# Kernel optimization log

Hardware: AMD Instinct MI355X
Metric: run time of the kernel (lower is better)

Reference implementation:

```python
import jax, jax.numpy as jnp
import numpy as np

B, S, E, H = 4, 2048, 1024, 16
D = E // H  # head_size = 64

def setup_inputs() -> dict:
    key = jax.random.key(0)
    ks = jax.random.split(key, 10)
    s_e = E ** -0.5
    s_4e = (4 * E) ** -0.5
    inp = {
        "x": jax.random.normal(ks[0], (B, S, E), dtype=jnp.float32),
        # per-head Q/K/V weights, stacked: [H, E, D], no bias
        "Wq": jax.random.normal(ks[1], (H, E, D), dtype=jnp.float32) * s_e,
        "Wk": jax.random.normal(ks[2], (H, E, D), dtype=jnp.float32) * s_e,
        "Wv": jax.random.normal(ks[3], (H, E, D), dtype=jnp.float32) * s_e,
        "Wo": jax.random.normal(ks[4], (E, E), dtype=jnp.float32) * s_e,
        "bo": jax.random.normal(ks[5], (E,), dtype=jnp.float32) * 0.01,
        "W1": jax.random.normal(ks[6], (E, 4 * E), dtype=jnp.float32) * s_e,
        "b1": jax.random.normal(ks[7], (4 * E,), dtype=jnp.float32) * 0.01,
        "W2": jax.random.normal(ks[8], (4 * E, E), dtype=jnp.float32) * s_4e,
        "b2": jax.random.normal(ks[9], (E,), dtype=jnp.float32) * 0.01,
    }
    return inp

def reference(x, Wq, Wk, Wv, Wo, bo, W1, b1, W2, b2):
    b, s, e = x.shape
    # NOTE: original scales by embedding_size**-0.5 (Size of x), not head_size
    scale = e ** -0.5
    q = jnp.einsum("bse,hed->bhsd", x, Wq)
    k = jnp.einsum("bse,hed->bhsd", x, Wk)
    v = jnp.einsum("bse,hed->bhsd", x, Wv)
    scores = jnp.einsum("bhsd,bhtd->bhst", q, k) * scale
    causal = jnp.tril(jnp.ones((s, s), dtype=bool))
    scores = jnp.where(causal, scores, -jnp.inf)
    weights = jax.nn.softmax(scores, axis=-1)
    attn = jnp.einsum("bhst,bhtd->bhsd", weights, v)  # [B,H,S,D]
    # concat heads along last dim: [B,S,H*D]
    attn = attn.transpose(0, 2, 1, 3).reshape(b, s, e)
    y = attn @ Wo + bo
    x = x + y  # residual (no LayerNorm applied in original forward)
    h = jax.nn.relu(x @ W1 + b1)
    ffn = h @ W2 + b2
    return x + ffn
```

## Files before the change

kernel.cpp:

```cpp
#include <hip/hip_runtime.h>
#include <stdint.h>

#define B_ 4
#define S_ 2048
#define E_ 1024
#define H_ 16
#define D_ 64

typedef unsigned short u16;
typedef u16 u16x8 __attribute__((ext_vector_type(8)));
typedef __bf16 bf16x8 __attribute__((ext_vector_type(8)));
typedef float f32x4 __attribute__((ext_vector_type(4)));

__device__ __forceinline__ float bf2f(u16 x) {
  unsigned int v = ((unsigned int)x) << 16;
  return __builtin_bit_cast(float, v);
}
__device__ __forceinline__ u16 f2bf(float f) {
  unsigned int u = __builtin_bit_cast(unsigned int, f);
  unsigned int r = (u + 0x7fffu + ((u >> 16) & 1u)) >> 16;
  return (u16)r;
}

__device__ __forceinline__ void gl2lds16(const u16* g, u16* l) {
  __builtin_amdgcn_global_load_lds(
      (const __attribute__((address_space(1))) void*)g,
      (__attribute__((address_space(3))) void*)l, 16, 0, 0);
}

__global__ __launch_bounds__(256) void cast_bf16_k(const float* __restrict__ src,
                                                   u16* __restrict__ dst, long n) {
  long i = ((long)blockIdx.x * 256 + threadIdx.x) * 8;
  if (i + 8 <= n) {
    f32x4 a = *(const f32x4*)(src + i), b = *(const f32x4*)(src + i + 4);
    u16x8 o;
#pragma unroll
    for (int j = 0; j < 4; j++) { o[j] = f2bf(a[j]); o[j + 4] = f2bf(b[j]); }
    *(u16x8*)(dst + i) = o;
  }
}

__global__ __launch_bounds__(256) void castT_k(const float* __restrict__ src,
                                               u16* __restrict__ dst, int R, int C) {
  long bofs = (long)blockIdx.z * R * C;
  src += bofs; dst += bofs;
  __shared__ u16 t[32][33];
  int c0 = blockIdx.x * 32, r0 = blockIdx.y * 32;
  int lc = threadIdx.x & 31, lr8 = threadIdx.x >> 5;
#pragma unroll
  for (int i = 0; i < 4; i++) {
    int lr = lr8 + i * 8;
    t[lr][lc] = f2bf(src[(long)(r0 + lr) * C + c0 + lc]);
  }
  __syncthreads();
#pragma unroll
  for (int i = 0; i < 4; i++) {
    int lr = lr8 + i * 8;
    dst[(long)(c0 + lr) * R + r0 + lc] = t[lc][lr];
  }
}

__global__ __launch_bounds__(256) void vT_k(const u16* __restrict__ QKV,
                                            u16* __restrict__ VTg) {
  int bh = blockIdx.z, d0 = blockIdx.y * 32, t0 = blockIdx.x * 32;
  int b = bh >> 4, h = bh & 15;
  __shared__ u16 t[32][33];
  int lc = threadIdx.x & 31, lr8 = threadIdx.x >> 5;
#pragma unroll
  for (int i = 0; i < 4; i++) {
    int lr = lr8 + i * 8;
    t[lr][lc] = QKV[(long)(b * S_ + t0 + lr) * 3072 + 2048 + h * 64 + d0 + lc];
  }
  __syncthreads();
#pragma unroll
  for (int i = 0; i < 4; i++) {
    int lr = lr8 + i * 8;
    VTg[((long)bh * 64 + d0 + lr) * S_ + t0 + lc] = t[lc][lr];
  }
}

template <bool AF32, bool CF32>
__global__ __launch_bounds__(256) void gemm128(const void* __restrict__ Av,
                                               const u16* __restrict__ BT,
                                               void* __restrict__ Cv,
                                               const float* __restrict__ bias,
                                               const float* __restrict__ resid,
                                               int M, int N, int K, int relu,
                                               u16* __restrict__ Cbf) {
  __shared__ u16 As[128 * 32];
  __shared__ u16 Bs[128 * 32];
  const int tid = threadIdx.x;
  const int wave = tid >> 6, lane = tid & 63;
  const int m0 = blockIdx.y * 128, n0 = blockIdx.x * 128;
  const int wm = wave >> 1, wn = wave & 1;
  const int fr = lane & 15, quad = lane >> 4;

  f32x4 acc[4][4] = {};

  const int srow = wave * 32 + (lane >> 2);
  const int skcol = (lane & 3) * 8;

  for (int k0 = 0; k0 < K; k0 += 32) {
    __syncthreads();
    if (AF32) {
      const float* Ap = (const float*)Av + (long)(m0 + (tid >> 1)) * K + k0 + (tid & 1) * 16;
      f32x4 f0 = *(const f32x4*)Ap, f1 = *(const f32x4*)(Ap + 4);
      f32x4 f2 = *(const f32x4*)(Ap + 8), f3 = *(const f32x4*)(Ap + 12);
      u16x8 p0, p1;
#pragma unroll
      for (int j = 0; j < 4; j++) {
        p0[j] = f2bf(f0[j]); p0[j + 4] = f2bf(f1[j]);
        p1[j] = f2bf(f2[j]); p1[j + 4] = f2bf(f3[j]);
      }
      *(u16x8*)&As[(tid >> 1) * 32 + (tid & 1) * 16] = p0;
      *(u16x8*)&As[(tid >> 1) * 32 + (tid & 1) * 16 + 8] = p1;
    } else {
      const u16* Ag = (const u16*)Av + (long)(m0 + srow) * K + k0 + skcol;
      gl2lds16(Ag, &As[(wave * 32) * 32]);
      gl2lds16(Ag + 16 * (long)K, &As[(wave * 32 + 16) * 32]);
    }
    {
      const u16* Bg = BT + (long)(n0 + srow) * K + k0 + skcol;
      gl2lds16(Bg, &Bs[(wave * 32) * 32]);
      gl2lds16(Bg + 16 * (long)K, &Bs[(wave * 32 + 16) * 32]);
    }
    __syncthreads();

    bf16x8 af[4], bfr[4];
#pragma unroll
    for (int mi = 0; mi < 4; mi++)
      af[mi] = __builtin_bit_cast(bf16x8, *(const u16x8*)&As[(wm * 64 + mi * 16 + fr) * 32 + quad * 8]);
#pragma unroll
    for (int ni = 0; ni < 4; ni++)
      bfr[ni] = __builtin_bit_cast(bf16x8, *(const u16x8*)&Bs[(wn * 64 + ni * 16 + fr) * 32 + quad * 8]);
#pragma unroll
    for (int mi = 0; mi < 4; mi++)
#pragma unroll
      for (int ni = 0; ni < 4; ni++)
        acc[mi][ni] = __builtin_amdgcn_mfma_f32_16x16x32_bf16(af[mi], bfr[ni], acc[mi][ni], 0, 0, 0);
  }

#pragma unroll
  for (int mi = 0; mi < 4; mi++)
#pragma unroll
    for (int ni = 0; ni < 4; ni++)
#pragma unroll
      for (int r = 0; r < 4; r++) {
        int gm = m0 + wm * 64 + mi * 16 + quad * 4 + r;
        int gn = n0 + wn * 64 + ni * 16 + fr;
        float v = acc[mi][ni][r];
        if (bias) v += bias[gn];
        if (resid) v += resid[(long)gm * N + gn];
        if (relu) v = fmaxf(v, 0.f);
        if (CF32) ((float*)Cv)[(long)gm * N + gn] = v;
        else      ((u16*)Cv)[(long)gm * N + gn] = f2bf(v);
        if (Cbf) Cbf[(long)gm * N + gn] = f2bf(v);
      }
}

__device__ __forceinline__ bf16x8 ldfrag32(const u16* base, int r, int quad) {
  int u = (r * 32 + quad * 8) ^ (((r >> 3) & 1) << 4);
  return __builtin_bit_cast(bf16x8, *(const u16x8*)(base + u));
}

__device__ __forceinline__ void stage_tile(const u16* __restrict__ A,
                                           const u16* __restrict__ BT, int K,
                                           int m0, int n0, int k0,
                                           u16* __restrict__ buf,
                                           int sr_, int sc_, int wbase) {
#pragma unroll
  for (int h = 0; h < 2; h++) {
    int r = h * 128 + sr_;
    int c = sc_ ^ (((r >> 3) & 1) << 4);
    gl2lds16(A + (size_t)(m0 + r) * K + k0 + c, buf + h * 4096 + wbase);
  }
  int c = sc_ ^ (((sr_ >> 3) & 1) << 4);
  gl2lds16(BT + (size_t)(n0 + sr_) * K + k0 + c, buf + 8192 + wbase);
}

template <bool CF32>
__global__ __launch_bounds__(512) void gemm3b(const u16* __restrict__ A,
                                              const u16* __restrict__ BT,
                                              void* __restrict__ Cv,
                                              const float* __restrict__ bias,
                                              const float* __restrict__ resid,
                                              int M, int N, int K, int relu,
                                              u16* __restrict__ Cbf) {
  (void)M;
  constexpr int BM = 256, BN = 128, BK = 32;
  constexpr int AU = BM * BK;
  constexpr int BUF = AU + BN * BK;

  __shared__ u16 sm[3 * BUF];
  const int tid = threadIdx.x;
  const int wave = tid >> 6, lane = tid & 63;
  const int wm = wave >> 1, wn = wave & 1;
  const int fr = lane & 15, quad = lane >> 4;

  const int nbx = gridDim.x;
  const int nwg = nbx * (int)gridDim.y;
  const int wgid = blockIdx.y * nbx + blockIdx.x;
  const int qq = nwg >> 3, rr = nwg & 7;
  const int xcd = wgid & 7, loc = wgid >> 3;
  const int sw = (xcd < rr ? xcd * (qq + 1) : rr * (qq + 1) + (xcd - rr) * qq) + loc;
  const int n0 = (sw % nbx) * BN;
  const int m0 = (sw / nbx) * BM;

  const int NT = K / BK;

  f32x4 acc[4][4] = {};

  const int sc_ = (tid & 3) * 8;
  const int sr_ = tid >> 2;
  const int wbase = wave << 9;

  const int rA = wm * 64 + fr;
  const int rB = wn * 64 + fr;

  stage_tile(A, BT, K, m0, n0, 0, sm, sr_, sc_, wbase);
  if (NT > 1) {
    stage_tile(A, BT, K, m0, n0, BK, sm + BUF, sr_, sc_, wbase);
    asm volatile("s_waitcnt vmcnt(3)" ::: "memory");
  } else {
    asm volatile("s_waitcnt vmcnt(0)" ::: "memory");
  }
  __builtin_amdgcn_s_barrier();

  int cur = 0;
  for (int t = 0; t < NT; ++t) {
    u16* cb = sm + cur * BUF;

    if (t + 2 < NT) {
      int s2 = cur + 2; if (s2 >= 3) s2 -= 3;
      stage_tile(A, BT, K, m0, n0, (t + 2) * BK, sm + s2 * BUF, sr_, sc_, wbase);
    }

    bf16x8 aF[4], bF[4];
#pragma unroll
    for (int mi = 0; mi < 4; ++mi) aF[mi] = ldfrag32(cb, rA + mi * 16, quad);
#pragma unroll
    for (int ni = 0; ni < 4; ++ni) bF[ni] = ldfrag32(cb + AU, rB + ni * 16, quad);

    asm volatile("s_waitcnt lgkmcnt(0)" ::: "memory");
    __builtin_amdgcn_sched_barrier(0);
    __builtin_amdgcn_s_setprio(1);
#pragma unroll
    for (int mi = 0; mi < 4; ++mi)
#pragma unroll
      for (int ni = 0; ni < 4; ++ni)
        acc[mi][ni] = __builtin_amdgcn_mfma_f32_16x16x32_bf16(aF[mi], bF[ni], acc[mi][ni], 0, 0, 0);
    __builtin_amdgcn_s_setprio(0);

    if (t + 2 < NT) asm volatile("s_waitcnt vmcnt(3)" ::: "memory");
    else            asm volatile("s_waitcnt vmcnt(0)" ::: "memory");
    __builtin_amdgcn_s_barrier();
    cur = cur + 1; if (cur >= 3) cur -= 3;
  }

#pragma unroll
  for (int mi = 0; mi < 4; ++mi)
#pragma unroll
    for (int ni = 0; ni < 4; ++ni)
#pragma unroll
      for (int r = 0; r < 4; ++r) {
        int gm = m0 + wm * 64 + mi * 16 + quad * 4 + r;
        int gn = n0 + wn * 64 + ni * 16 + fr;
        float v = acc[mi][ni][r];
        if (bias) v += bias[gn];
        if (resid) v += resid[(long)gm * N + gn];
        if (relu) v = fmaxf(v, 0.f);
        if (CF32) ((float*)Cv)[(long)gm * N + gn] = v;
        else      ((u16*)Cv)[(long)gm * N + gn] = f2bf(v);
        if (Cbf) Cbf[(long)gm * N + gn] = f2bf(v);
      }
}

__device__ __forceinline__ void stage_tile_s(const u16* __restrict__ A,
                                             const u16* __restrict__ BT, int K,
                                             int m0, int n0, int k0,
                                             u16* __restrict__ buf,
                                             int sr_, int sc_, int wbase) {
#pragma unroll
  for (int h = 0; h < 2; h++) {
    int r = h * 64 + sr_;
    int c = sc_ ^ (((r >> 3) & 1) << 4);
    gl2lds16(A + (size_t)(m0 + r) * K + k0 + c, buf + h * 2048 + wbase);
  }
#pragma unroll
  for (int h = 0; h < 2; h++) {
    int r = h * 64 + sr_;
    int c = sc_ ^ (((r >> 3) & 1) << 4);
    gl2lds16(BT + (size_t)(n0 + r) * K + k0 + c, buf + 4096 + h * 2048 + wbase);
  }
}

template <bool CF32>
__global__ __launch_bounds__(256) void gemm3s(const u16* __restrict__ A,
                                              const u16* __restrict__ BT,
                                              void* __restrict__ Cv,
                                              const float* __restrict__ bias,
                                              const float* __restrict__ resid,
                                              int M, int N, int K, int relu,
                                              u16* __restrict__ Cbf) {
  (void)M;
  constexpr int BM = 128, BN = 128, BK = 32;
  constexpr int AU = BM * BK;
  constexpr int BUF = 2 * AU;

  __shared__ u16 sm[3 * BUF];
  const int tid = threadIdx.x;
  const int wave = tid >> 6, lane = tid & 63;
  const int wm = wave >> 1, wn = wave & 1;
  const int fr = lane & 15, quad = lane >> 4;

  const int nbx = gridDim.x;
  const int nwg = nbx * (int)gridDim.y;
  const int wgid = blockIdx.y * nbx + blockIdx.x;
  const int qq = nwg >> 3, rr = nwg & 7;
  const int xcd = wgid & 7, loc = wgid >> 3;
  const int sw = (xcd < rr ? xcd * (qq + 1) : rr * (qq + 1) + (xcd - rr) * qq) + loc;
  const int n0 = (sw % nbx) * BN;
  const int m0 = (sw / nbx) * BM;

  const int NT = K / BK;

  f32x4 acc[4][4] = {};

  const int sc_ = (tid & 3) * 8;
  const int sr_ = tid >> 2;
  const int wbase = wave << 9;

  const int rA = wm * 64 + fr;
  const int rB = wn * 64 + fr;

  stage_tile_s(A, BT, K, m0, n0, 0, sm, sr_, sc_, wbase);
  if (NT > 1) {
    stage_tile_s(A, BT, K, m0, n0, BK, sm + BUF, sr_, sc_, wbase);
    asm volatile("s_waitcnt vmcnt(4)" ::: "memory");
  } else {
    asm volatile("s_waitcnt vmcnt(0)" ::: "memory");
  }
  __builtin_amdgcn_s_barrier();

  int cur = 0;
  for (int t = 0; t < NT; ++t) {
    u16* cb = sm + cur * BUF;

    if (t + 2 < NT) {
      int s2 = cur + 2; if (s2 >= 3) s2 -= 3;
      stage_tile_s(A, BT, K, m0, n0, (t + 2) * BK, sm + s2 * BUF, sr_, sc_, wbase);
    }

    bf16x8 aF[4], bF[4];
#pragma unroll
    for (int mi = 0; mi < 4; ++mi) aF[mi] = ldfrag32(cb, rA + mi * 16, quad);
#pragma unroll
    for (int ni = 0; ni < 4; ++ni) bF[ni] = ldfrag32(cb + AU, rB + ni * 16, quad);

    asm volatile("s_waitcnt lgkmcnt(0)" ::: "memory");
    __builtin_amdgcn_sched_barrier(0);
    __builtin_amdgcn_s_setprio(1);
#pragma unroll
    for (int mi = 0; mi < 4; ++mi)
#pragma unroll
      for (int ni = 0; ni < 4; ++ni)
        acc[mi][ni] = __builtin_amdgcn_mfma_f32_16x16x32_bf16(aF[mi], bF[ni], acc[mi][ni], 0, 0, 0);
    __builtin_amdgcn_s_setprio(0);

    if (t + 2 < NT) asm volatile("s_waitcnt vmcnt(4)" ::: "memory");
    else            asm volatile("s_waitcnt vmcnt(0)" ::: "memory");
    __builtin_amdgcn_s_barrier();
    cur = cur + 1; if (cur >= 3) cur -= 3;
  }

#pragma unroll
  for (int mi = 0; mi < 4; ++mi)
#pragma unroll
    for (int ni = 0; ni < 4; ++ni)
#pragma unroll
      for (int r = 0; r < 4; ++r) {
        int gm = m0 + wm * 64 + mi * 16 + quad * 4 + r;
        int gn = n0 + wn * 64 + ni * 16 + fr;
        float v = acc[mi][ni][r];
        if (bias) v += bias[gn];
        if (resid) v += resid[(long)gm * N + gn];
        if (relu) v = fmaxf(v, 0.f);
        if (CF32) ((float*)Cv)[(long)gm * N + gn] = v;
        else      ((u16*)Cv)[(long)gm * N + gn] = f2bf(v);
        if (Cbf) Cbf[(long)gm * N + gn] = f2bf(v);
      }
}

#define SWZ(row, col) ((((row) << 6)) + ((col) ^ (((row) & 7) << 3)))

__global__ __launch_bounds__(256) void attn_mfma3(const u16* __restrict__ QKV,
                                                  const u16* __restrict__ VTg,
                                                  u16* __restrict__ attn) {
  int p = blockIdx.x, h = blockIdx.y, b = blockIdx.z;
  int tid = threadIdx.x;
  int wq = tid >> 6, lane = tid & 63;
  int fr = lane & 15, quad = lane >> 4;
  int kf = quad * 8;

  __shared__ u16 Qs[64 * 64];
  __shared__ u16 Ks[64 * 64];
  __shared__ u16 Vt[64 * 64];
  __shared__ u16 Ps[4 * 16 * 64];

  const u16* base = QKV + (long)b * S_ * 3072;
  const u16* vbase = VTg + (long)(b * 16 + h) * 64 * S_;
  int st = tid >> 2;
  int sd = (tid & 3) * 16;

  const float qsc = 0.03125f * 1.4426950408889634f;

  for (int ti = 0; ti < 2; ti++) {
    int qt = ti ? (31 - p) : p;

    {
      const u16* qr = base + (long)(qt * 64 + st) * 3072 + h * 64 + sd;
      u16x8 a = *(const u16x8*)qr, d = *(const u16x8*)(qr + 8);
      u16x8 oa, od;
#pragma unroll
      for (int j = 0; j < 8; j++) {
        oa[j] = f2bf(bf2f(a[j]) * qsc);
        od[j] = f2bf(bf2f(d[j]) * qsc);
      }
      *(u16x8*)&Qs[SWZ(st, sd)] = oa;
      *(u16x8*)&Qs[SWZ(st, sd + 8)] = od;
    }
    __syncthreads();
    bf16x8 qf0 = __builtin_bit_cast(bf16x8, *(const u16x8*)&Qs[SWZ(wq * 16 + fr, kf)]);
    bf16x8 qf1 = __builtin_bit_cast(bf16x8, *(const u16x8*)&Qs[SWZ(wq * 16 + fr, 32 + kf)]);

    f32x4 acc[4] = {};
    float l[4] = {0.f, 0.f, 0.f, 0.f};

    for (int c = 0; c <= qt; c++) {
      int t0 = c * 64;
      __syncthreads();
      {
        const u16* kr = base + (long)(t0 + st) * 3072 + 1024 + h * 64 + sd;
        u16x8 k0 = *(const u16x8*)kr, k1 = *(const u16x8*)(kr + 8);
        const u16* vr = vbase + (long)st * S_ + t0 + sd;
        u16x8 v0 = *(const u16x8*)vr, v1 = *(const u16x8*)(vr + 8);
        *(u16x8*)&Ks[SWZ(st, sd)] = k0;
        *(u16x8*)&Ks[SWZ(st, sd + 8)] = k1;
        *(u16x8*)&Vt[SWZ(st, sd)] = v0;
        *(u16x8*)&Vt[SWZ(st, sd + 8)] = v1;
      }
      __syncthreads();

      f32x4 sc[4] = {};
#pragma unroll
      for (int nt = 0; nt < 4; nt++) {
        bf16x8 b0 = __builtin_bit_cast(bf16x8, *(const u16x8*)&Ks[SWZ(nt * 16 + fr, kf)]);
        bf16x8 b1 = __builtin_bit_cast(bf16x8, *(const u16x8*)&Ks[SWZ(nt * 16 + fr, 32 + kf)]);
        sc[nt] = __builtin_amdgcn_mfma_f32_16x16x32_bf16(qf0, b0, sc[nt], 0, 0, 0);
        sc[nt] = __builtin_amdgcn_mfma_f32_16x16x32_bf16(qf1, b1, sc[nt], 0, 0, 0);
      }

      if (c == qt) {
        int qloc = wq * 16 + quad * 4;
#pragma unroll
        for (int nt = 0; nt < 4; nt++)
#pragma unroll
          for (int r = 0; r < 4; r++)
            if (nt * 16 + fr > qloc + r) sc[nt][r] = -1e30f;
      }

      const int pb = wq << 10;
      const int prow = quad * 4;
#pragma unroll
      for (int nt = 0; nt < 4; nt++) {
        int col = nt * 16 + fr;
#pragma unroll
        for (int r = 0; r < 4; r++) {
          float pv = exp2f(sc[nt][r]);
          l[r] += pv;
          Ps[pb + SWZ(prow + r, col)] = f2bf(pv);
        }
      }

      bf16x8 pa0 = __builtin_bit_cast(bf16x8, *(const u16x8*)&Ps[pb + SWZ(fr, kf)]);
      bf16x8 pa1 = __builtin_bit_cast(bf16x8, *(const u16x8*)&Ps[pb + SWZ(fr, 32 + kf)]);
#pragma unroll
      for (int nt = 0; nt < 4; nt++) {
        bf16x8 vb0 = __builtin_bit_cast(bf16x8, *(const u16x8*)&Vt[SWZ(nt * 16 + fr, kf)]);
        bf16x8 vb1 = __builtin_bit_cast(bf16x8, *(const u16x8*)&Vt[SWZ(nt * 16 + fr, 32 + kf)]);
        acc[nt] = __builtin_amdgcn_mfma_f32_16x16x32_bf16(pa0, vb0, acc[nt], 0, 0, 0);
        acc[nt] = __builtin_amdgcn_mfma_f32_16x16x32_bf16(pa1, vb1, acc[nt], 0, 0, 0);
      }
    }

#pragma unroll
    for (int r = 0; r < 4; r++)
#pragma unroll
      for (int off = 1; off < 16; off <<= 1) l[r] += __shfl_xor(l[r], off);

    long row = (long)b * S_ + qt * 64 + wq * 16 + quad * 4;
#pragma unroll
    for (int nt = 0; nt < 4; nt++)
#pragma unroll
      for (int r = 0; r < 4; r++)
        attn[(row + r) * 1024 + h * 64 + nt * 16 + fr] = f2bf(acc[nt][r] / l[r]);
  }
}

extern "C" void kernel_launch(void* const* d_in, const int* in_sizes, int n_in,
                              void* d_out, int out_size, void* d_ws, size_t ws_size,
                              hipStream_t stream) {
  (void)in_sizes; (void)n_in; (void)out_size;
  const float* x  = (const float*)d_in[0];
  const float* Wq = (const float*)d_in[1];
  const float* Wk = (const float*)d_in[2];
  const float* Wv = (const float*)d_in[3];
  const float* Wo = (const float*)d_in[4];
  const float* bo = (const float*)d_in[5];
  const float* W1 = (const float*)d_in[6];
  const float* b1 = (const float*)d_in[7];
  const float* W2 = (const float*)d_in[8];
  const float* b2 = (const float*)d_in[9];
  float* out = (float*)d_out;

  char* ws = (char*)d_ws;
  u16*   QKV  = (u16*)(ws);
  u16*   attn = (u16*)(ws + 50331648);
  u16*   hbuf = (u16*)(ws);
  float* x1   = (float*)(ws + 67108864);
  u16*   VTg  = (u16*)(ws + 67108864);
  u16*   xb   = (u16*)(ws + 83886080);
  u16*   WT   = (u16*)(ws + 100663296);
  u16*   WoT  = (u16*)(ws + 106954752);
  u16*   W1T  = (u16*)(ws + 109051904);
  u16*   W2T  = (u16*)(ws + 117440512);
  u16*   x1b  = (u16*)(ws + 125829120);
  bool bigws = ws_size >= (size_t)142606336;

  cast_bf16_k<<<4096, 256, 0, stream>>>(x, xb, (long)8192 * 1024);
  castT_k<<<dim3(2, 32, 16), 256, 0, stream>>>(Wq, WT, 1024, 64);
  castT_k<<<dim3(2, 32, 16), 256, 0, stream>>>(Wk, WT + 1048576, 1024, 64);
  castT_k<<<dim3(2, 32, 16), 256, 0, stream>>>(Wv, WT + 2097152, 1024, 64);
  castT_k<<<dim3(32, 32, 1), 256, 0, stream>>>(Wo, WoT, 1024, 1024);
  castT_k<<<dim3(128, 32, 1), 256, 0, stream>>>(W1, W1T, 1024, 4096);
  castT_k<<<dim3(32, 128, 1), 256, 0, stream>>>(W2, W2T, 4096, 1024);

  gemm3s<false><<<dim3(24, 64), 256, 0, stream>>>(xb, WT, QKV, nullptr, nullptr, 8192, 3072, 1024, 0, nullptr);
  vT_k<<<dim3(64, 2, 64), 256, 0, stream>>>(QKV, VTg);
  attn_mfma3<<<dim3(16, H_, B_), 256, 0, stream>>>(QKV, VTg, attn);
  gemm3s<true><<<dim3(8, 64), 256, 0, stream>>>(attn, WoT, x1, bo, x, 8192, 1024, 1024, 0, bigws ? x1b : nullptr);
  if (bigws)
    gemm3b<false><<<dim3(32, 32), 512, 0, stream>>>(x1b, W1T, hbuf, b1, nullptr, 8192, 4096, 1024, 1, nullptr);
  else
    gemm128<true, false><<<dim3(32, 64), 256, 0, stream>>>(x1, W1T, hbuf, b1, nullptr, 8192, 4096, 1024, 1, nullptr);
  gemm3s<true><<<dim3(8, 64), 256, 0, stream>>>(hbuf, W2T, out, b2, x1, 8192, 1024, 4096, 0, nullptr);
}
```

Measured before the change: 569.1 us.

## Use 256x256 GEMM tiles, 256-row tiles elsewhere, padded LDS in attention

Adds a 512-thread GEMM variant with 256x256 block tiles and uses it for the QKV and W1 projections. The Wo and W2 projections move onto the existing 256x128 512-thread kernel. The attention kernel switches from an XOR-swizzled LDS layout to row padding, and from exp2f with the log2e factor folded into Q to __expf. Larger tiles raise operand reuse per block and cut redundant global loads, but they leave fewer blocks per launch, which can hurt wave quantization. The QKV launch, for example, has 384 blocks.

```diff
diff --git a/kernel.cpp b/kernel.cpp
--- a/kernel.cpp
+++ b/kernel.cpp
@@ -275,27 +275,27 @@
       }
 }
 
-__device__ __forceinline__ void stage_tile_s(const u16* __restrict__ A,
+__device__ __forceinline__ void stage_tile_w(const u16* __restrict__ A,
                                              const u16* __restrict__ BT, int K,
                                              int m0, int n0, int k0,
                                              u16* __restrict__ buf,
                                              int sr_, int sc_, int wbase) {
 #pragma unroll
   for (int h = 0; h < 2; h++) {
-    int r = h * 64 + sr_;
+    int r = h * 128 + sr_;
     int c = sc_ ^ (((r >> 3) & 1) << 4);
-    gl2lds16(A + (size_t)(m0 + r) * K + k0 + c, buf + h * 2048 + wbase);
+    gl2lds16(A + (size_t)(m0 + r) * K + k0 + c, buf + h * 4096 + wbase);
   }
 #pragma unroll
   for (int h = 0; h < 2; h++) {
-    int r = h * 64 + sr_;
+    int r = h * 128 + sr_;
     int c = sc_ ^ (((r >> 3) & 1) << 4);
-    gl2lds16(BT + (size_t)(n0 + r) * K + k0 + c, buf + 4096 + h * 2048 + wbase);
+    gl2lds16(BT + (size_t)(n0 + r) * K + k0 + c, buf + 8192 + h * 4096 + wbase);
   }
 }
 
 template <bool CF32>
-__global__ __launch_bounds__(256) void gemm3s(const u16* __restrict__ A,
+__global__ __launch_bounds__(512) void gemm3w(const u16* __restrict__ A,
                                               const u16* __restrict__ BT,
                                               void* __restrict__ Cv,
                                               const float* __restrict__ bias,
@@ -303,14 +303,14 @@
                                               int M, int N, int K, int relu,
                                               u16* __restrict__ Cbf) {
   (void)M;
-  constexpr int BM = 128, BN = 128, BK = 32;
+  constexpr int BM = 256, BN = 256, BK = 32;
   constexpr int AU = BM * BK;
   constexpr int BUF = 2 * AU;
 
   __shared__ u16 sm[3 * BUF];
   const int tid = threadIdx.x;
   const int wave = tid >> 6, lane = tid & 63;
-  const int wm = wave >> 1, wn = wave & 1;
+  const int wm = wave >> 2, wn = wave & 3;
   const int fr = lane & 15, quad = lane >> 4;
 
   const int nbx = gridDim.x;
@@ -324,18 +324,18 @@
 
   const int NT = K / BK;
 
-  f32x4 acc[4][4] = {};
+  f32x4 acc[8][4] = {};
 
   const int sc_ = (tid & 3) * 8;
   const int sr_ = tid >> 2;
   const int wbase = wave << 9;
 
-  const int rA = wm * 64 + fr;
+  const int rA = wm * 128 + fr;
   const int rB = wn * 64 + fr;
 
-  stage_tile_s(A, BT, K, m0, n0, 0, sm, sr_, sc_, wbase);
+  stage_tile_w(A, BT, K, m0, n0, 0, sm, sr_, sc_, wbase);
   if (NT > 1) {
-    stage_tile_s(A, BT, K, m0, n0, BK, sm + BUF, sr_, sc_, wbase);
+    stage_tile_w(A, BT, K, m0, n0, BK, sm + BUF, sr_, sc_, wbase);
     asm volatile("s_waitcnt vmcnt(4)" ::: "memory");
   } else {
     asm volatile("s_waitcnt vmcnt(0)" ::: "memory");
@@ -348,12 +348,12 @@
 
     if (t + 2 < NT) {
       int s2 = cur + 2; if (s2 >= 3) s2 -= 3;
-      stage_tile_s(A, BT, K, m0, n0, (t + 2) * BK, sm + s2 * BUF, sr_, sc_, wbase);
+      stage_tile_w(A, BT, K, m0, n0, (t + 2) * BK, sm + s2 * BUF, sr_, sc_, wbase);
     }
 
-    bf16x8 aF[4], bF[4];
-#pragma unroll
-    for (int mi = 0; mi < 4; ++mi) aF[mi] = ldfrag32(cb, rA + mi * 16, quad);
+    bf16x8 aF[8], bF[4];
+#pragma unroll
+    for (int mi = 0; mi < 8; ++mi) aF[mi] = ldfrag32(cb, rA + mi * 16, quad);
 #pragma unroll
     for (int ni = 0; ni < 4; ++ni) bF[ni] = ldfrag32(cb + AU, rB + ni * 16, quad);
 
@@ -361,7 +361,7 @@
     __builtin_amdgcn_sched_barrier(0);
     __builtin_amdgcn_s_setprio(1);
 #pragma unroll
-    for (int mi = 0; mi < 4; ++mi)
+    for (int mi = 0; mi < 8; ++mi)
 #pragma unroll
       for (int ni = 0; ni < 4; ++ni)
         acc[mi][ni] = __builtin_amdgcn_mfma_f32_16x16x32_bf16(aF[mi], bF[ni], acc[mi][ni], 0, 0, 0);
@@ -374,12 +374,12 @@
   }
 
 #pragma unroll
-  for (int mi = 0; mi < 4; ++mi)
+  for (int mi = 0; mi < 8; ++mi)
 #pragma unroll
     for (int ni = 0; ni < 4; ++ni)
 #pragma unroll
       for (int r = 0; r < 4; ++r) {
-        int gm = m0 + wm * 64 + mi * 16 + quad * 4 + r;
+        int gm = m0 + wm * 128 + mi * 16 + quad * 4 + r;
         int gn = n0 + wn * 64 + ni * 16 + fr;
         float v = acc[mi][ni][r];
         if (bias) v += bias[gn];
@@ -391,8 +391,6 @@
       }
 }
 
-#define SWZ(row, col) ((((row) << 6)) + ((col) ^ (((row) & 7) << 3)))
-
 __global__ __launch_bounds__(256) void attn_mfma3(const u16* __restrict__ QKV,
                                                   const u16* __restrict__ VTg,
                                                   u16* __restrict__ attn) {
@@ -402,18 +400,16 @@
   int fr = lane & 15, quad = lane >> 4;
   int kf = quad * 8;
 
-  __shared__ u16 Qs[64 * 64];
-  __shared__ u16 Ks[64 * 64];
-  __shared__ u16 Vt[64 * 64];
-  __shared__ u16 Ps[4 * 16 * 64];
+  __shared__ u16 Qs[64][72];
+  __shared__ u16 Ks[64][72];
+  __shared__ u16 Vt[64][72];
+  __shared__ u16 Ps[4][16][72];
 
   const u16* base = QKV + (long)b * S_ * 3072;
   const u16* vbase = VTg + (long)(b * 16 + h) * 64 * S_;
   int st = tid >> 2;
   int sd = (tid & 3) * 16;
 
-  const float qsc = 0.03125f * 1.4426950408889634f;
-
   for (int ti = 0; ti < 2; ti++) {
     int qt = ti ? (31 - p) : p;
 
@@ -423,15 +419,15 @@
       u16x8 oa, od;
 #pragma unroll
       for (int j = 0; j < 8; j++) {
-        oa[j] = f2bf(bf2f(a[j]) * qsc);
-        od[j] = f2bf(bf2f(d[j]) * qsc);
-      }
-      *(u16x8*)&Qs[SWZ(st, sd)] = oa;
-      *(u16x8*)&Qs[SWZ(st, sd + 8)] = od;
+        oa[j] = f2bf(bf2f(a[j]) * 0.03125f);
+        od[j] = f2bf(bf2f(d[j]) * 0.03125f);
+      }
+      *(u16x8*)&Qs[st][sd] = oa;
+      *(u16x8*)&Qs[st][sd + 8] = od;
     }
     __syncthreads();
-    bf16x8 qf0 = __builtin_bit_cast(bf16x8, *(const u16x8*)&Qs[SWZ(wq * 16 + fr, kf)]);
-    bf16x8 qf1 = __builtin_bit_cast(bf16x8, *(const u16x8*)&Qs[SWZ(wq * 16 + fr, 32 + kf)]);
+    bf16x8 qf0 = __builtin_bit_cast(bf16x8, *(const u16x8*)&Qs[wq * 16 + fr][kf]);
+    bf16x8 qf1 = __builtin_bit_cast(bf16x8, *(const u16x8*)&Qs[wq * 16 + fr][32 + kf]);
 
     f32x4 acc[4] = {};
     float l[4] = {0.f, 0.f, 0.f, 0.f};
@@ -444,18 +440,18 @@
         u16x8 k0 = *(const u16x8*)kr, k1 = *(const u16x8*)(kr + 8);
         const u16* vr = vbase + (long)st * S_ + t0 + sd;
         u16x8 v0 = *(const u16x8*)vr, v1 = *(const u16x8*)(vr + 8);
-        *(u16x8*)&Ks[SWZ(st, sd)] = k0;
-        *(u16x8*)&Ks[SWZ(st, sd + 8)] = k1;
-        *(u16x8*)&Vt[SWZ(st, sd)] = v0;
-        *(u16x8*)&Vt[SWZ(st, sd + 8)] = v1;
+        *(u16x8*)&Ks[st][sd] = k0;
+        *(u16x8*)&Ks[st][sd + 8] = k1;
+        *(u16x8*)&Vt[st][sd] = v0;
+        *(u16x8*)&Vt[st][sd + 8] = v1;
       }
       __syncthreads();
 
       f32x4 sc[4] = {};
 #pragma unroll
       for (int nt = 0; nt < 4; nt++) {
-        bf16x8 b0 = __builtin_bit_cast(bf16x8, *(const u16x8*)&Ks[SWZ(nt * 16 + fr, kf)]);
-        bf16x8 b1 = __builtin_bit_cast(bf16x8, *(const u16x8*)&Ks[SWZ(nt * 16 + fr, 32 + kf)]);
+        bf16x8 b0 = __builtin_bit_cast(bf16x8, *(const u16x8*)&Ks[nt * 16 + fr][kf]);
+        bf16x8 b1 = __builtin_bit_cast(bf16x8, *(const u16x8*)&Ks[nt * 16 + fr][32 + kf]);
         sc[nt] = __builtin_amdgcn_mfma_f32_16x16x32_bf16(qf0, b0, sc[nt], 0, 0, 0);
         sc[nt] = __builtin_amdgcn_mfma_f32_16x16x32_bf16(qf1, b1, sc[nt], 0, 0, 0);
       }
@@ -469,25 +465,27 @@
             if (nt * 16 + fr > qloc + r) sc[nt][r] = -1e30f;
       }
 
-      const int pb = wq << 10;
-      const int prow = quad * 4;
+#pragma unroll
+      for (int nt = 0; nt < 4; nt++)
+#pragma unroll
+        for (int r = 0; r < 4; r++) {
+          float pv = __expf(sc[nt][r]);
+          sc[nt][r] = pv;
+          l[r] += pv;
+        }
+
+#pragma unroll
+      for (int nt = 0; nt < 4; nt++)
+#pragma unroll
+        for (int r = 0; r < 4; r++)
+          Ps[wq][quad * 4 + r][nt * 16 + fr] = f2bf(sc[nt][r]);
+
+      bf16x8 pa0 = __builtin_bit_cast(bf16x8, *(const u16x8*)&Ps[wq][fr][kf]);
+      bf16x8 pa1 = __builtin_bit_cast(bf16x8, *(const u16x8*)&Ps[wq][fr][32 + kf]);
 #pragma unroll
       for (int nt = 0; nt < 4; nt++) {
-        int col = nt * 16 + fr;
-#pragma unroll
-        for (int r = 0; r < 4; r++) {
-          float pv = exp2f(sc[nt][r]);
-          l[r] += pv;
-          Ps[pb + SWZ(prow + r, col)] = f2bf(pv);
-        }
-      }
-
-      bf16x8 pa0 = __builtin_bit_cast(bf16x8, *(const u16x8*)&Ps[pb + SWZ(fr, kf)]);
-      bf16x8 pa1 = __builtin_bit_cast(bf16x8, *(const u16x8*)&Ps[pb + SWZ(fr, 32 + kf)]);
-#pragma unroll
-      for (int nt = 0; nt < 4; nt++) {
-        bf16x8 vb0 = __builtin_bit_cast(bf16x8, *(const u16x8*)&Vt[SWZ(nt * 16 + fr, kf)]);
-        bf16x8 vb1 = __builtin_bit_cast(bf16x8, *(const u16x8*)&Vt[SWZ(nt * 16 + fr, 32 + kf)]);
+        bf16x8 vb0 = __builtin_bit_cast(bf16x8, *(const u16x8*)&Vt[nt * 16 + fr][kf]);
+        bf16x8 vb1 = __builtin_bit_cast(bf16x8, *(const u16x8*)&Vt[nt * 16 + fr][32 + kf]);
         acc[nt] = __builtin_amdgcn_mfma_f32_16x16x32_bf16(pa0, vb0, acc[nt], 0, 0, 0);
         acc[nt] = __builtin_amdgcn_mfma_f32_16x16x32_bf16(pa1, vb1, acc[nt], 0, 0, 0);
       }
@@ -545,13 +543,13 @@
   castT_k<<<dim3(128, 32, 1), 256, 0, stream>>>(W1, W1T, 1024, 4096);
   castT_k<<<dim3(32, 128, 1), 256, 0, stream>>>(W2, W2T, 4096, 1024);
 
-  gemm3s<false><<<dim3(24, 64), 256, 0, stream>>>(xb, WT, QKV, nullptr, nullptr, 8192, 3072, 1024, 0, nullptr);
+  gemm3w<false><<<dim3(12, 32), 512, 0, stream>>>(xb, WT, QKV, nullptr, nullptr, 8192, 3072, 1024, 0, nullptr);
   vT_k<<<dim3(64, 2, 64), 256, 0, stream>>>(QKV, VTg);
   attn_mfma3<<<dim3(16, H_, B_), 256, 0, stream>>>(QKV, VTg, attn);
-  gemm3s<true><<<dim3(8, 64), 256, 0, stream>>>(attn, WoT, x1, bo, x, 8192, 1024, 1024, 0, bigws ? x1b : nullptr);
+  gemm3b<true><<<dim3(8, 32), 512, 0, stream>>>(attn, WoT, x1, bo, x, 8192, 1024, 1024, 0, bigws ? x1b : nullptr);
   if (bigws)
-    gemm3b<false><<<dim3(32, 32), 512, 0, stream>>>(x1b, W1T, hbuf, b1, nullptr, 8192, 4096, 1024, 1, nullptr);
+    gemm3w<false><<<dim3(16, 32), 512, 0, stream>>>(x1b, W1T, hbuf, b1, nullptr, 8192, 4096, 1024, 1, nullptr);
   else
     gemm128<true, false><<<dim3(32, 64), 256, 0, stream>>>(x1, W1T, hbuf, b1, nullptr, 8192, 4096, 1024, 1, nullptr);
-  gemm3s<true><<<dim3(8, 64), 256, 0, stream>>>(hbuf, W2T, out, b2, x1, 8192, 1024, 4096, 0, nullptr);
-}
+  gemm3b<true><<<dim3(8, 32), 512, 0, stream>>>(hbuf, W2T, out, b2, x1, 8192, 1024, 4096, 0, nullptr);
+}
```

Result: faster. 553.6 us (-2.7%).
